# Kernel optimization log

Hardware: AMD Instinct MI355X
Metric: run time of the kernel (lower is better)

Reference implementation:

```python
import jax, jax.numpy as jnp
import numpy as np

B, S, NSAMP = 64, 21, 3000
HID, SEC, N, ATT = 500, 6, 2, 128
OUT, NPROTO, NCLS, NHEAD = 128, 25, 5, 4


def _pe(length, d):
    pos = np.arange(length, dtype=np.float32)[:, None]
    div = np.exp(np.arange(0, d, 2, dtype=np.float32) * (-np.log(10000.0) / d))
    pe = np.zeros((length, d), np.float32)
    pe[:, 0::2] = np.sin(pos * div)
    pe[:, 1::2] = np.cos(pos * div)
    return jnp.asarray(pe)


def _ln(x, g, b, eps=1e-5):
    m = x.mean(-1, keepdims=True)
    v = ((x - m) ** 2).mean(-1, keepdims=True)
    return (x - m) * jax.lax.rsqrt(v + eps) * g + b


def _conv1d(x, w, b):
    y = jax.lax.conv_general_dilated(x, w, (1,), [(1, 1)], dimension_numbers=('NCH', 'OIH', 'NCH'))
    return y + b[None, :, None]


def _maxpool(x, k):
    n, c, l = x.shape
    m = (l // k) * k  # torch MaxPool1d floors
    return x[:, :, :m].reshape(n, c, l // k, k).max(-1)


def _bn_eval(x, g, b, eps=1e-5):
    # eval-mode BatchNorm1d with running_mean=0, running_var=1
    return x * (g / np.sqrt(1.0 + eps))[None, :, None] + b[None, :, None]


def setup_inputs():
    key = jax.random.key(0)
    ks = jax.random.split(key, 16)
    def w(i, shape, s=0.02):
        return jax.random.normal(ks[i], shape, jnp.float32) * s
    u = jax.random.uniform(ks[0], (B * S * N, SEC), jnp.float32, 1e-6, 1.0 - 1e-6)
    return dict(
        x=jax.random.normal(ks[1], (B, S, 1, NSAMP), jnp.float32),
        gumbel=-jnp.log(-jnp.log(u)),
        wq=w(2, (HID, ATT * N)), wk=w(3, (HID, ATT * N)),
        w1=w(4, (32, 1, 3)), b1=jnp.zeros(32), bn1_g=jnp.ones(32), bn1_b=jnp.zeros(32),
        w2=w(5, (64, 32, 3)), b2=jnp.zeros(64), bn2_g=jnp.ones(64), bn2_b=jnp.zeros(64),
        w3=w(6, (128, 64, 3)), b3=jnp.zeros(128), bn3_g=jnp.ones(128), bn3_b=jnp.zeros(128),
        fc_w=w(7, (768, 256)), fc_b=jnp.zeros(256),
        fc2_w=w(8, (256, OUT)), fc2_b=jnp.zeros(OUT),
        protos=w(9, (NPROTO, OUT), 1.0),
        in_w=w(10, (OUT, 3 * OUT)), in_b=jnp.zeros(3 * OUT),
        out_w=w(11, (OUT, OUT)), out_b=jnp.zeros(OUT),
        ln1_g=jnp.ones(OUT), ln1_b=jnp.zeros(OUT),
        ln2_g=jnp.ones(OUT), ln2_b=jnp.zeros(OUT),
        ff1_w=w(12, (OUT, OUT)), ff1_b=jnp.zeros(OUT),
        ff2_w=w(13, (OUT, OUT)), ff2_b=jnp.zeros(OUT),
        clf_w=w(14, (OUT, NCLS)), clf_b=jnp.zeros(NCLS),
    )


def reference(x, gumbel, wq, wk, w1, b1, bn1_g, bn1_b, w2, b2, bn2_g, bn2_b,
              w3, b3, bn3_g, bn3_b, fc_w, fc_b, fc2_w, fc2_b, protos,
              in_w, in_b, out_w, out_b, ln1_g, ln1_b, ln2_g, ln2_b,
              ff1_w, ff1_b, ff2_w, ff2_b, clf_w, clf_b):
    bs = B * S
    # ---- HardAttentionLayer (gumbel hard sampling over SEC sections) ----
    xr = x.reshape(bs, SEC, HID)                       # (BS, 6, 500)
    xp = xr + _pe(100, HID)[None, :SEC]
    q = (xp @ wq).reshape(bs, SEC, N, ATT).transpose(0, 2, 1, 3)  # bnsh
    k = (xp @ wk).reshape(bs, SEC, N, ATT).transpose(0, 2, 1, 3)
    att = jnp.einsum('bnsh,bnth->bnst', q, k) / (HID ** 0.5)
    logits = (att.sum(-1) / SEC).reshape(bs * N, SEC)
    y_soft = jax.nn.softmax(logits + gumbel)           # tau = 1.0
    y_hard = jax.nn.one_hot(jnp.argmax(y_soft, -1), SEC, dtype=y_soft.dtype)
    alphas = (y_hard - jax.lax.stop_gradient(y_soft) + y_soft).reshape(bs, N, SEC)
    sampled = jnp.einsum('bns,bsh->bnh', alphas, xr)   # (BS, N, 500)
    # ---- conv/MLP epoch encoder (eval: dropout off, BN running stats) ----
    c = sampled.reshape(bs * N, 1, HID)
    c = _bn_eval(_maxpool(jax.nn.relu(_conv1d(c, w1, b1)), 4), bn1_g, bn1_b)
    c = _bn_eval(_maxpool(jax.nn.relu(_conv1d(c, w2, b2)), HID // 100), bn2_g, bn2_b)
    c = _bn_eval(_maxpool(jax.nn.relu(_conv1d(c, w3, b3)), 4), bn3_g, bn3_b)
    c = c.reshape(bs * N, -1) @ fc_w + fc_b
    z = c @ fc2_w + fc2_b                              # (B*S*N, 128)
    # ---- PrototypeLayer: VQ codebook lookup with straight-through ----
    d2 = (z * z).sum(1, keepdims=True) + (protos * protos).sum(1) - 2.0 * z @ protos.T
    proto = protos[jnp.argmin(d2, 1)]
    proto_st = z + jax.lax.stop_gradient(proto - z)
    # ---- SequenceEncoder: 1-layer post-norm transformer ----
    p_clf = proto_st.reshape(B, S, N, OUT).sum(2) / N  # (B, S, 128)
    h = p_clf + _pe(1024, OUT)[None, :S]
    qkv = h @ in_w + in_b
    qh, kh, vh = [t.reshape(B, S, NHEAD, OUT // NHEAD) for t in jnp.split(qkv, 3, -1)]
    sc = jnp.einsum('bqhd,bkhd->bhqk', qh, kh) / ((OUT // NHEAD) ** 0.5)
    ctx = jnp.einsum('bhqk,bkhd->bqhd', jax.nn.softmax(sc, -1), vh).reshape(B, S, OUT)
    h = _ln(h + ctx @ out_w + out_b, ln1_g, ln1_b)
    ff = jax.nn.relu(h @ ff1_w + ff1_b) @ ff2_w + ff2_b
    h = _ln(h + ff, ln2_g, ln2_b)
    return (h.reshape(-1, OUT) @ clf_w + clf_b).reshape(B, S, NCLS)
```

## Files before the change

### kernel.cpp

```cpp
#include <hip/hip_runtime.h>
#include <math.h>

#define BB 64
#define SS 21
#define NSAMP 3000
#define HID 500
#define SECN 6
#define NN 2
#define OUTD 128
#define NPROTO 25
#define NCLS 5
#define NHEAD 4
#define BS (BB*SS)
#define NSAMPLE (BS*NN)

#define C500 (-0.0184206807439523674f)
#define C128 (-0.07195578415606439f)
#define LSCALE 0.00745355992499929898f

#define WS_W2HI 5376
#define WS_W2LO 8448
#define WS_W3HI 11520
#define WS_W3LO 23808
#define WS_P3   36096
#define WS_C3   55296
#define WS_WQT  55424
#define WS_V    727424
#define WS_QKV  WS_V
#define WS_CTX  (WS_V + 520192)

typedef __attribute__((ext_vector_type(8))) short short8;
typedef __attribute__((ext_vector_type(4))) float floatx4;

__device__ __forceinline__ short f2bf(float f) {
  unsigned u = __float_as_uint(f);
  u += 0x7FFF + ((u >> 16) & 1);
  return (short)(u >> 16);
}
__device__ __forceinline__ float bf2f(short h) {
  return __uint_as_float(((unsigned)(unsigned short)h) << 16);
}

__global__ __launch_bounds__(256) void prep_all_kernel(
    const float* __restrict__ w2, const float* __restrict__ w3,
    short* __restrict__ w2hi, short* __restrict__ w2lo,
    short* __restrict__ w3hi, short* __restrict__ w3lo,
    const float* __restrict__ protos, const float* __restrict__ fc2w,
    const float* __restrict__ fcw, const float* __restrict__ fcb,
    const float* __restrict__ fc2b,
    float* __restrict__ P3, float* __restrict__ c3,
    const float* __restrict__ wq, float* __restrict__ wqT) {
  __shared__ __align__(16) float p2row[256];
  __shared__ float red[256];
  __shared__ float tile[64][65];
  const int t = threadIdx.x;
  if (blockIdx.x < 120) {
    int idx = blockIdx.x * 256 + t;
    if (idx < 6144) {
      int ic = idx & 31, ck = idx >> 5, k = ck % 3, c = ck / 3;
      float v = w2[c * 96 + ic * 3 + k];
      int dst = (((k * 4 + (c >> 4)) * 64) + ((ic >> 3) * 16 + (c & 15))) * 8 + (ic & 7);
      short hi = f2bf(v);
      short lo = f2bf(v - bf2f(hi));
      w2hi[dst] = hi; w2lo[dst] = lo;
    } else if (idx < 30720) {
      int j = idx - 6144;
      int ic = j & 63, ck = j >> 6, k = ck % 3, c = ck / 3;
      float v = w3[(c * 64 + ic) * 3 + k];
      int s = k * 2 + (ic >> 5);
      int dst = (((s * 8 + (c >> 4)) * 64) + (((ic & 31) >> 3) * 16 + (c & 15))) * 8 + (ic & 7);
      short hi = f2bf(v);
      short lo = f2bf(v - bf2f(hi));
      w3hi[dst] = hi; w3lo[dst] = lo;
    }
    return;
  }
  if (blockIdx.x >= 145) {
    int tid = blockIdx.x - 145;
    int h0 = (tid >> 2) * 64, c0 = (tid & 3) * 64;
    for (int e = t; e < 4096; e += 256) {
      int i = e >> 6, j = e & 63;
      if (h0 + i < 500) tile[j][i] = wq[(h0 + i) * 256 + c0 + j];
    }
    __syncthreads();
    for (int e = t; e < 4096; e += 256) {
      int c = e >> 6, hh = e & 63;
      if (h0 + hh < 500) wqT[(c0 + c) * 500 + h0 + hh] = tile[c][hh];
    }
    return;
  }
  const int p = blockIdx.x - 120, j = t;
  {
    const float4* pr = reinterpret_cast<const float4*>(protos + p * 128);
    const float4* wr = reinterpret_cast<const float4*>(fc2w + j * 128);
    float4 a4 = make_float4(0.f, 0.f, 0.f, 0.f);
    for (int c4 = 0; c4 < 32; c4++) {
      float4 a = pr[c4], b = wr[c4];
      a4.x += a.x * b.x; a4.y += a.y * b.y; a4.z += a.z * b.z; a4.w += a.w * b.w;
    }
    float v = (a4.x + a4.y) + (a4.z + a4.w);
    p2row[j] = v;
    float contrib = v * fcb[j];
    if (j < 128) {
      float pv = protos[p * 128 + j];
      contrib += pv * fc2b[j] - 0.5f * pv * pv;
    }
    red[j] = contrib;
  }
  __syncthreads();
  for (int s = 128; s > 0; s >>= 1) {
    if (j < s) red[j] += red[j + s];
    __syncthreads();
  }
  if (j == 0) c3[p] = red[0];
  for (int k = j; k < 768; k += 256) {
    const float4* fr = reinterpret_cast<const float4*>(fcw + k * 256);
    const float4* p2 = reinterpret_cast<const float4*>(p2row);
    float4 a4 = make_float4(0.f, 0.f, 0.f, 0.f);
    for (int j4 = 0; j4 < 64; j4++) {
      float4 a = p2[j4], b = fr[j4];
      a4.x += a.x * b.x; a4.y += a.y * b.y; a4.z += a.z * b.z; a4.w += a.w * b.w;
    }
    P3[p * 768 + k] = (a4.x + a4.y) + (a4.z + a4.w);
  }
}

#define MBX 4
__global__ __launch_bounds__(512) void attn_b_kernel(
    const float* __restrict__ x, const float* __restrict__ wk,
    const float* __restrict__ wqT, float* __restrict__ v) {
  __shared__ __align__(16) float pesum[500];
  __shared__ __align__(16) float xs[MBX * 500];
  __shared__ __align__(16) float ksp[2 * 256 * MBX];
  __shared__ __align__(16) float ks_t[256 * MBX];
  const int blk = blockIdx.x, t = threadIdx.x;

  if (t < 125) {
    float div0 = expf((float)(4 * t) * C500);
    float div1 = expf((float)(4 * t + 2) * C500);
    float s0 = 0.f, c0 = 0.f, s1 = 0.f, c1 = 0.f;
#pragma unroll
    for (int s = 0; s < SECN; s++) {
      float a0 = (float)s * div0, a1 = (float)s * div1;
      s0 += sinf(a0); c0 += cosf(a0);
      s1 += sinf(a1); c1 += cosf(a1);
    }
    reinterpret_cast<float4*>(pesum)[t] = make_float4(s0, c0, s1, c1);
  }
  __syncthreads();

  for (int e = t; e < MBX * 125; e += 512) {
    int m = e / 125, h4 = e % 125;
    const float4* xr = reinterpret_cast<const float4*>(x) + (blk * MBX + m) * 750;
    float4 a = xr[h4];
#pragma unroll
    for (int s = 1; s < SECN; s++) {
      float4 b = xr[s * 125 + h4];
      a.x += b.x; a.y += b.y; a.z += b.z; a.w += b.w;
    }
    float4 pe = reinterpret_cast<float4*>(pesum)[h4];
    a.x += pe.x; a.y += pe.y; a.z += pe.z; a.w += pe.w;
    reinterpret_cast<float4*>(xs)[m * 125 + h4] = a;
  }
  __syncthreads();

  {
    int c = t & 255, kh = t >> 8;
    float acc[MBX];
#pragma unroll
    for (int m = 0; m < MBX; m++) acc[m] = 0.f;
    int b4 = kh ? 63 : 0, e4 = kh ? 125 : 63;
    const float4* xsb = reinterpret_cast<const float4*>(xs);
    for (int i4 = b4; i4 < e4; i4++) {
      int i = i4 * 4;
      float w0 = wk[(i + 0) * 256 + c];
      float w1 = wk[(i + 1) * 256 + c];
      float w2 = wk[(i + 2) * 256 + c];
      float w3 = wk[(i + 3) * 256 + c];
#pragma unroll
      for (int m = 0; m < MBX; m++) {
        float4 xv = xsb[m * 125 + i4];
        acc[m] += xv.x * w0 + xv.y * w1 + xv.z * w2 + xv.w * w3;
      }
    }
#pragma unroll
    for (int m = 0; m < MBX; m++)
      ksp[(kh * 256 + c) * MBX + m] = acc[m];
  }
  __syncthreads();
  for (int e = t; e < 256 * MBX; e += 512) ks_t[e] = ksp[e] + ksp[256 * MBX + e];
  __syncthreads();

  if (t < 500) {
    int h = t;
#pragma unroll
    for (int n = 0; n < 2; n++) {
      float acc[MBX];
#pragma unroll
      for (int m = 0; m < MBX; m++) acc[m] = 0.f;
      const float* wcol = wqT + (n * 128) * 500 + h;
      const floatx4* ktb = (const floatx4*)ks_t + n * 128;
      for (int c = 0; c < 128; c++) {
        float w = wcol[c * 500];
        floatx4 k0 = ktb[c];
        acc[0] += w * k0[0]; acc[1] += w * k0[1]; acc[2] += w * k0[2]; acc[3] += w * k0[3];
      }
#pragma unroll
      for (int m = 0; m < MBX; m++)
        v[((blk * MBX + m) * 2 + n) * 500 + h] = acc[m];
    }
  }
}

__global__ __launch_bounds__(192) void attn_c_kernel(
    const float* __restrict__ x, const float* __restrict__ v,
    const float* __restrict__ gumbel, int* __restrict__ sec_idx) {
  __shared__ float lgsh[NN][SECN];
  const int bs = blockIdx.x, t = threadIdx.x;
  const int s = t >> 5, lane = t & 31;
  const float4* x4 = reinterpret_cast<const float4*>(x) + bs * 750 + s * 125;
  const float4* v0 = reinterpret_cast<const float4*>(v) + bs * 250;
  const float4* v1 = v0 + 125;
  float a0 = 0.f, a1 = 0.f;
  for (int h4 = lane; h4 < 125; h4 += 32) {
    float4 xv = x4[h4];
    float div0 = expf((float)(4 * h4) * C500);
    float div1 = expf((float)(4 * h4 + 2) * C500);
    float ang0 = (float)s * div0, ang1 = (float)s * div1;
    xv.x += sinf(ang0); xv.y += cosf(ang0);
    xv.z += sinf(ang1); xv.w += cosf(ang1);
    float4 w0 = v0[h4], w1 = v1[h4];
    a0 += xv.x * w0.x + xv.y * w0.y + xv.z * w0.z + xv.w * w0.w;
    a1 += xv.x * w1.x + xv.y * w1.y + xv.z * w1.z + xv.w * w1.w;
  }
#pragma unroll
  for (int m = 16; m >= 1; m >>= 1) {
    a0 += __shfl_xor(a0, m);
    a1 += __shfl_xor(a1, m);
  }
  if (lane == 0) {
    lgsh[0][s] = a0 * LSCALE + gumbel[(bs * 2 + 0) * SECN + s];
    lgsh[1][s] = a1 * LSCALE + gumbel[(bs * 2 + 1) * SECN + s];
  }
  __syncthreads();
  if (t < 2) {
    int best = 0; float bv = lgsh[t][0];
    for (int i = 1; i < SECN; i++) {
      float q = lgsh[t][i];
      if (q > bv) { bv = q; best = i; }
    }
    sec_idx[bs * 2 + t] = best;
  }
}

#define CONV_LDS 53568
__global__ __launch_bounds__(256, 3) void conv_kernel(
    const float* __restrict__ x, const int* __restrict__ sec_idx,
    const float* __restrict__ w1, const float* __restrict__ b1,
    const float* __restrict__ bn1g, const float* __restrict__ bn1b,
    const short* __restrict__ w2hi, const short* __restrict__ w2lo,
    const float* __restrict__ b2,
    const float* __restrict__ bn2g, const float* __restrict__ bn2b,
    const short* __restrict__ w3hi, const short* __restrict__ w3lo,
    const float* __restrict__ b3,
    const float* __restrict__ bn3g, const float* __restrict__ bn3b,
    const float* __restrict__ P3, const float* __restrict__ c3,
    int* __restrict__ proto_idx) {
  __shared__ __align__(16) char smem[CONV_LDS];
  short* act1_hi  = (short*)smem;
  short* act1_lo  = (short*)(smem + 10400);
  short* act2p_hi = (short*)smem;
  short* act2p_lo = (short*)(smem + 4896);
  float* featsh   = (float*)(smem + 9792);
  float* sc25     = (float*)(smem + 12864);
  float* in0p  = (float*)(smem + 20800);
  float* act2t = (float*)(smem + 20800);
  float* act3t = (float*)(smem + 20800);

  const int sample = blockIdx.x;
  const int t = threadIdx.x;
  const int bsIdx = sample >> 1;
  const float bnscale = rsqrtf(1.0f + 1e-5f);
  const int wv = t >> 6, l = t & 63, lr = l & 15, lg2 = l >> 4;

  {
    int sec = sec_idx[sample];
    const float* src = &x[bsIdx * NSAMP + sec * HID];
    for (int i = t; i < 512; i += 256) in0p[i] = (i >= 1 && i <= 500) ? src[i - 1] : 0.f;
    if (t < 200) {
      int r = t / 40; r = (r == 0) ? 0 : 125 + r;
      int idx = r * 40 + t % 40;
      act1_hi[idx] = 0; act1_lo[idx] = 0;
    }
  }
  __syncthreads();

  {
    int ic = t & 31;
    float w0 = w1[ic * 3], w1v = w1[ic * 3 + 1], w2v = w1[ic * 3 + 2];
    float bb = b1[ic];
    float g = bn1g[ic] * bnscale, be = bn1b[ic];
    for (int p = t >> 5; p < 125; p += 8) {
      int base = 4 * p;
      float xm1 = in0p[base], x0 = in0p[base + 1], x1 = in0p[base + 2],
            x2 = in0p[base + 3], x3 = in0p[base + 4], x4 = in0p[base + 5];
      float a0 = bb + w0 * xm1 + w1v * x0 + w2v * x1;
      float a1 = bb + w0 * x0  + w1v * x1 + w2v * x2;
      float a2 = bb + w0 * x1  + w1v * x2 + w2v * x3;
      float a3 = bb + w0 * x2  + w1v * x3 + w2v * x4;
      float m = fmaxf(fmaxf(fmaxf(fmaxf(a0, a1), a2), a3), 0.f);
      float v = m * g + be;
      short hi = f2bf(v);
      short lo = f2bf(v - bf2f(hi));
      act1_hi[(p + 1) * 40 + ic] = hi;
      act1_lo[(p + 1) * 40 + ic] = lo;
    }
  }
  __syncthreads();

  {
    floatx4 acc[4][2];
#pragma unroll
    for (int m = 0; m < 4; m++)
#pragma unroll
      for (int nn = 0; nn < 2; nn++) acc[m][nn] = (floatx4){0.f, 0.f, 0.f, 0.f};
#pragma unroll
    for (int s = 0; s < 3; s++) {
      short8 Ah[4], Al[4], Bh[2], Bl[2];
#pragma unroll
      for (int m = 0; m < 4; m++) {
        int aoff = ((s * 4 + m) * 64 + l) * 8;
        Ah[m] = *(const short8*)(w2hi + aoff);
        Al[m] = *(const short8*)(w2lo + aoff);
      }
#pragma unroll
      for (int nn = 0; nn < 2; nn++) {
        int boff = ((2 * wv + nn) * 16 + lr + s) * 40 + lg2 * 8;
        Bh[nn] = *(const short8*)(act1_hi + boff);
        Bl[nn] = *(const short8*)(act1_lo + boff);
      }
#pragma unroll
      for (int m = 0; m < 4; m++)
#pragma unroll
        for (int nn = 0; nn < 2; nn++) {
          acc[m][nn] = __builtin_amdgcn_mfma_f32_16x16x32_bf16(Ah[m], Bh[nn], acc[m][nn], 0, 0, 0);
          acc[m][nn] = __builtin_amdgcn_mfma_f32_16x16x32_bf16(Ah[m], Bl[nn], acc[m][nn], 0, 0, 0);
          acc[m][nn] = __builtin_amdgcn_mfma_f32_16x16x32_bf16(Al[m], Bh[nn], acc[m][nn], 0, 0, 0);
        }
    }
#pragma unroll
    for (int m = 0; m < 4; m++)
#pragma unroll
      for (int nn = 0; nn < 2; nn++) {
        int p = (2 * wv + nn) * 16 + lr;
        int swz = (m * 4 + lg2) ^ lr;
        *(floatx4*)(act2t + p * 64 + swz * 4) = acc[m][nn];
      }
  }
  __syncthreads();

  {
    if (t < 162) {
      for (int i = t; i < 648; i += 162) {
        int r = i / 72; r = (r == 0) ? 0 : 25 + r;
        int idx = r * 72 + i % 72;
        act2p_hi[idx] = 0; act2p_lo[idx] = 0;
      }
    }
    int ic = t & 63;
    float bb = b2[ic], g = bn2g[ic] * bnscale, be = bn2b[ic];
#define A2T(r, c) act2t[(r) * 64 + ((((c) >> 2) ^ ((r) & 15)) << 2) + ((c) & 3)]
    for (int pw = t >> 6; pw < 25; pw += 4) {
      int base = 5 * pw;
      float m = A2T(base, ic);
      m = fmaxf(m, A2T(base + 1, ic));
      m = fmaxf(m, A2T(base + 2, ic));
      m = fmaxf(m, A2T(base + 3, ic));
      m = fmaxf(m, A2T(base + 4, ic));
      float v = fmaxf(m + bb, 0.f) * g + be;
      short hi = f2bf(v);
      short lo = f2bf(v - bf2f(hi));
      act2p_hi[(pw + 1) * 72 + ic] = hi;
      act2p_lo[(pw + 1) * 72 + ic] = lo;
    }
#undef A2T
  }
  __syncthreads();

  {
    floatx4 acc[2][2];
#pragma unroll
    for (int mm = 0; mm < 2; mm++)
#pragma unroll
      for (int nn = 0; nn < 2; nn++) acc[mm][nn] = (floatx4){0.f, 0.f, 0.f, 0.f};
#pragma unroll
    for (int s = 0; s < 6; s++) {
      short8 Ah[2], Al[2], Bh[2], Bl[2];
#pragma unroll
      for (int mm = 0; mm < 2; mm++) {
        int aoff = ((s * 8 + (wv * 2 + mm)) * 64 + l) * 8;
        Ah[mm] = *(const short8*)(w3hi + aoff);
        Al[mm] = *(const short8*)(w3lo + aoff);
      }
#pragma unroll
      for (int nn = 0; nn < 2; nn++) {
        int boff = (nn * 16 + lr + (s >> 1)) * 72 + (s & 1) * 32 + lg2 * 8;
        Bh[nn] = *(const short8*)(act2p_hi + boff);
        Bl[nn] = *(const short8*)(act2p_lo + boff);
      }
#pragma unroll
      for (int mm = 0; mm < 2; mm++)
#pragma unroll
        for (int nn = 0; nn < 2; nn++) {
          acc[mm][nn] = __builtin_amdgcn_mfma_f32_16x16x32_bf16(Ah[mm], Bh[nn], acc[mm][nn], 0, 0, 0);
          acc[mm][nn] = __builtin_amdgcn_mfma_f32_16x16x32_bf16(Ah[mm], Bl[nn], acc[mm][nn], 0, 0, 0);
          acc[mm][nn] = __builtin_amdgcn_mfma_f32_16x16x32_bf16(Al[mm], Bh[nn], acc[mm][nn], 0, 0, 0);
        }
    }
#pragma unroll
    for (int mm = 0; mm < 2; mm++)
#pragma unroll
      for (int nn = 0; nn < 2; nn++) {
        int p = nn * 16 + lr;
        *(floatx4*)(act3t + p * 132 + (wv * 2 + mm) * 16 + lg2 * 4) = acc[mm][nn];
      }
  }
  __syncthreads();

  {
    int c = t & 127;
    float bb = b3[c], g = bn3g[c] * bnscale, be = bn3b[c];
    for (int pw = t >> 7; pw < 6; pw += 2) {
      int base = 4 * pw;
      float m = act3t[base * 132 + c];
      m = fmaxf(m, act3t[(base + 1) * 132 + c]);
      m = fmaxf(m, act3t[(base + 2) * 132 + c]);
      m = fmaxf(m, act3t[(base + 3) * 132 + c]);
      float v = fmaxf(m + bb, 0.f) * g + be;
      featsh[c * 6 + pw] = v;
    }
  }
  __syncthreads();

  if (t < NPROTO * 8) {
    int p = t >> 3, part = t & 7;
    const float4* pr = reinterpret_cast<const float4*>(P3 + p * 768 + part * 96);
    const float4* fr = reinterpret_cast<const float4*>(featsh + part * 96);
    float4 a4 = make_float4(0.f, 0.f, 0.f, 0.f);
#pragma unroll
    for (int i = 0; i < 24; i++) {
      float4 w = pr[i], f = fr[i];
      a4.x += w.x * f.x; a4.y += w.y * f.y; a4.z += w.z * f.z; a4.w += w.w * f.w;
    }
    float a = (a4.x + a4.y) + (a4.z + a4.w);
    a += __shfl_xor(a, 1);
    a += __shfl_xor(a, 2);
    a += __shfl_xor(a, 4);
    if (part == 0) sc25[p] = a + c3[p];
  }
  __syncthreads();
  if (t == 0) {
    int best = 0; float bv = sc25[0];
    for (int i = 1; i < NPROTO; i++) {
      float v = sc25[i];
      if (v > bv) { bv = v; best = i; }
    }
    proto_idx[sample] = best;
  }
}

__global__ __launch_bounds__(384) void seq_qkv_kernel(
    const int* __restrict__ proto_idx, const float* __restrict__ protos,
    const float* __restrict__ inw, const float* __restrict__ inb,
    float* __restrict__ qkv) {
  __shared__ __align__(16) float hrow[OUTD];
  const int bs = blockIdx.x, t = threadIdx.x;
  const int s = bs % SS;
  if (t < OUTD) {
    int i0 = proto_idx[bs * 2], i1 = proto_idx[bs * 2 + 1];
    float pc = 0.5f * (protos[i0 * OUTD + t] + protos[i1 * OUTD + t]);
    float div = expf((float)(2 * (t >> 1)) * C128);
    float ang = (float)s * div;
    float pe = (t & 1) ? cosf(ang) : sinf(ang);
    hrow[t] = pc + pe;
  }
  __syncthreads();
  float a = inb[t];
  const float4* hr = reinterpret_cast<const float4*>(hrow);
  for (int d4 = 0; d4 < 32; d4++) {
    float4 h4 = hr[d4];
    int d = d4 * 4;
    a += h4.x * inw[(d + 0) * 384 + t] + h4.y * inw[(d + 1) * 384 + t]
       + h4.z * inw[(d + 2) * 384 + t] + h4.w * inw[(d + 3) * 384 + t];
  }
  qkv[bs * 384 + t] = a;
}

__global__ __launch_bounds__(256) void seq_attn_kernel(
    const float* __restrict__ qkv, float* __restrict__ ctxbuf) {
  __shared__ float qs_[SS][32], ks_[SS][32], vs_[SS][32];
  __shared__ float sc_[SS][SS + 1];
  const int b = blockIdx.x >> 2, hd = blockIdx.x & 3;
  const int t = threadIdx.x;
  for (int e = t; e < SS * 32; e += 256) {
    int s = e >> 5, dd = e & 31;
    const float* base = qkv + (b * SS + s) * 384 + hd * 32 + dd;
    qs_[s][dd] = base[0];
    ks_[s][dd] = base[128];
    vs_[s][dd] = base[256];
  }
  __syncthreads();
  for (int e = t; e < SS * SS; e += 256) {
    int qs = e / SS, ks = e % SS;
    float a = 0.f;
#pragma unroll
    for (int d = 0; d < 32; d++) a += qs_[qs][d] * ks_[ks][d];
    sc_[qs][ks] = a * 0.17677669529663689f;
  }
  __syncthreads();
  if (t < SS) {
    float mx = sc_[t][0];
    for (int i = 1; i < SS; i++) mx = fmaxf(mx, sc_[t][i]);
    float sum = 0.f;
    for (int i = 0; i < SS; i++) { float e = expf(sc_[t][i] - mx); sc_[t][i] = e; sum += e; }
    float inv = 1.f / sum;
    for (int i = 0; i < SS; i++) sc_[t][i] *= inv;
  }
  __syncthreads();
  for (int e = t; e < SS * 32; e += 256) {
    int qs = e >> 5, dd = e & 31;
    float a = 0.f;
#pragma unroll
    for (int ks = 0; ks < SS; ks++) a += sc_[qs][ks] * vs_[ks][dd];
    ctxbuf[(b * SS + qs) * OUTD + hd * 32 + dd] = a;
  }
}

__global__ __launch_bounds__(128) void seq_tail_kernel(
    const int* __restrict__ proto_idx, const float* __restrict__ protos,
    const float* __restrict__ ctxbuf,
    const float* __restrict__ outw, const float* __restrict__ outb,
    const float* __restrict__ ln1g, const float* __restrict__ ln1b,
    const float* __restrict__ ff1w, const float* __restrict__ ff1b,
    const float* __restrict__ ff2w, const float* __restrict__ ff2b,
    const float* __restrict__ ln2g, const float* __restrict__ ln2b,
    const float* __restrict__ clfw, const float* __restrict__ clfb,
    float* __restrict__ out) {
  __shared__ __align__(16) float rowA[OUTD];
  __shared__ __align__(16) float rowB[OUTD];
  __shared__ float lds2[2];
  const int bs = blockIdx.x, t = threadIdx.x;
  const int s = bs % SS;

  rowA[t] = ctxbuf[bs * OUTD + t];
  __syncthreads();
  float a = outb[t];
  {
    const float4* cr = reinterpret_cast<const float4*>(rowA);
    for (int e4 = 0; e4 < 32; e4++) {
      float4 c4 = cr[e4];
      int e = e4 * 4;
      a += c4.x * outw[(e + 0) * OUTD + t] + c4.y * outw[(e + 1) * OUTD + t]
         + c4.z * outw[(e + 2) * OUTD + t] + c4.w * outw[(e + 3) * OUTD + t];
    }
  }
  float hv;
  {
    int i0 = proto_idx[bs * 2], i1 = proto_idx[bs * 2 + 1];
    float pc = 0.5f * (protos[i0 * OUTD + t] + protos[i1 * OUTD + t]);
    float div = expf((float)(2 * (t >> 1)) * C128);
    float ang = (float)s * div;
    float pe = (t & 1) ? cosf(ang) : sinf(ang);
    hv = pc + pe;
  }
  float tmp = hv + a;
  {
    float v = tmp;
#pragma unroll
    for (int k = 32; k >= 1; k >>= 1) v += __shfl_xor(v, k);
    if ((t & 63) == 0) lds2[t >> 6] = v;
    __syncthreads();
    float m = (lds2[0] + lds2[1]) * (1.0f / OUTD);
    __syncthreads();
    float u = tmp - m;
    float w = u * u;
#pragma unroll
    for (int k = 32; k >= 1; k >>= 1) w += __shfl_xor(w, k);
    if ((t & 63) == 0) lds2[t >> 6] = w;
    __syncthreads();
    float var = (lds2[0] + lds2[1]) * (1.0f / OUTD);
    __syncthreads();
    rowA[t] = u * rsqrtf(var + 1e-5f) * ln1g[t] + ln1b[t];
  }
  __syncthreads();
  {
    float r = ff1b[t];
    const float4* hr = reinterpret_cast<const float4*>(rowA);
    for (int e4 = 0; e4 < 32; e4++) {
      float4 h4 = hr[e4];
      int e = e4 * 4;
      r += h4.x * ff1w[(e + 0) * OUTD + t] + h4.y * ff1w[(e + 1) * OUTD + t]
         + h4.z * ff1w[(e + 2) * OUTD + t] + h4.w * ff1w[(e + 3) * OUTD + t];
    }
    rowB[t] = fmaxf(r, 0.f);
  }
  __syncthreads();
  float tmp2;
  {
    float r = ff2b[t];
    const float4* cr = reinterpret_cast<const float4*>(rowB);
    for (int e4 = 0; e4 < 32; e4++) {
      float4 c4 = cr[e4];
      int e = e4 * 4;
      r += c4.x * ff2w[(e + 0) * OUTD + t] + c4.y * ff2w[(e + 1) * OUTD + t]
         + c4.z * ff2w[(e + 2) * OUTD + t] + c4.w * ff2w[(e + 3) * OUTD + t];
    }
    tmp2 = rowA[t] + r;
  }
  __syncthreads();
  {
    float v = tmp2;
#pragma unroll
    for (int k = 32; k >= 1; k >>= 1) v += __shfl_xor(v, k);
    if ((t & 63) == 0) lds2[t >> 6] = v;
    __syncthreads();
    float m = (lds2[0] + lds2[1]) * (1.0f / OUTD);
    __syncthreads();
    float u = tmp2 - m;
    float w = u * u;
#pragma unroll
    for (int k = 32; k >= 1; k >>= 1) w += __shfl_xor(w, k);
    if ((t & 63) == 0) lds2[t >> 6] = w;
    __syncthreads();
    float var = (lds2[0] + lds2[1]) * (1.0f / OUTD);
    rowA[t] = u * rsqrtf(var + 1e-5f) * ln2g[t] + ln2b[t];
  }
  __syncthreads();
  if (t < NCLS) {
    float acc = clfb[t];
    for (int d = 0; d < OUTD; d++) acc += rowA[d] * clfw[d * NCLS + t];
    out[bs * NCLS + t] = acc;
  }
}

extern "C" void kernel_launch(void* const* d_in, const int* in_sizes, int n_in,
                              void* d_out, int out_size, void* d_ws, size_t ws_size,
                              hipStream_t stream) {
  const float* x     = (const float*)d_in[0];
  const float* gum   = (const float*)d_in[1];
  const float* wq    = (const float*)d_in[2];
  const float* wk    = (const float*)d_in[3];
  const float* w1    = (const float*)d_in[4];
  const float* b1    = (const float*)d_in[5];
  const float* bn1g  = (const float*)d_in[6];
  const float* bn1b  = (const float*)d_in[7];
  const float* w2    = (const float*)d_in[8];
  const float* b2    = (const float*)d_in[9];
  const float* bn2g  = (const float*)d_in[10];
  const float* bn2b  = (const float*)d_in[11];
  const float* w3    = (const float*)d_in[12];
  const float* b3    = (const float*)d_in[13];
  const float* bn3g  = (const float*)d_in[14];
  const float* bn3b  = (const float*)d_in[15];
  const float* fcw   = (const float*)d_in[16];
  const float* fcb   = (const float*)d_in[17];
  const float* fc2w  = (const float*)d_in[18];
  const float* fc2b  = (const float*)d_in[19];
  const float* prot  = (const float*)d_in[20];
  const float* inw   = (const float*)d_in[21];
  const float* inb   = (const float*)d_in[22];
  const float* outw  = (const float*)d_in[23];
  const float* outb  = (const float*)d_in[24];
  const float* ln1g  = (const float*)d_in[25];
  const float* ln1b  = (const float*)d_in[26];
  const float* ln2g  = (const float*)d_in[27];
  const float* ln2b  = (const float*)d_in[28];
  const float* ff1w  = (const float*)d_in[29];
  const float* ff1b  = (const float*)d_in[30];
  const float* ff2w  = (const float*)d_in[31];
  const float* ff2b  = (const float*)d_in[32];
  const float* clfw  = (const float*)d_in[33];
  const float* clfb  = (const float*)d_in[34];
  float* out = (float*)d_out;

  int* sec_idx   = (int*)d_ws;
  int* proto_idx = sec_idx + NSAMPLE;
  short* w2hi = (short*)((float*)d_ws + WS_W2HI);
  short* w2lo = (short*)((float*)d_ws + WS_W2LO);
  short* w3hi = (short*)((float*)d_ws + WS_W3HI);
  short* w3lo = (short*)((float*)d_ws + WS_W3LO);
  float* P3   = (float*)d_ws + WS_P3;
  float* c3   = (float*)d_ws + WS_C3;
  float* wqT  = (float*)d_ws + WS_WQT;
  float* vbuf = (float*)d_ws + WS_V;
  float* qkv  = (float*)d_ws + WS_QKV;
  float* ctxb = (float*)d_ws + WS_CTX;

  hipLaunchKernelGGL(prep_all_kernel, dim3(177), dim3(256), 0, stream,
                     w2, w3, w2hi, w2lo, w3hi, w3lo,
                     prot, fc2w, fcw, fcb, fc2b, P3, c3, wq, wqT);
  hipLaunchKernelGGL(attn_b_kernel, dim3(BS / MBX), dim3(512), 0, stream,
                     x, wk, wqT, vbuf);
  hipLaunchKernelGGL(attn_c_kernel, dim3(BS), dim3(192), 0, stream,
                     x, vbuf, gum, sec_idx);
  hipLaunchKernelGGL(conv_kernel, dim3(NSAMPLE), dim3(256), 0, stream,
                     x, sec_idx, w1, b1, bn1g, bn1b, w2hi, w2lo, b2, bn2g, bn2b,
                     w3hi, w3lo, b3, bn3g, bn3b, P3, c3, proto_idx);
  hipLaunchKernelGGL(seq_qkv_kernel, dim3(BS), dim3(384), 0, stream,
                     proto_idx, prot, inw, inb, qkv);
  hipLaunchKernelGGL(seq_attn_kernel, dim3(BB * NHEAD), dim3(256), 0, stream,
                     qkv, ctxb);
  hipLaunchKernelGGL(seq_tail_kernel, dim3(BS), dim3(128), 0, stream,
                     proto_idx, prot, ctxb, outw, outb, ln1g, ln1b,
                     ff1w, ff1b, ff2w, ff2b, ln2g, ln2b, clfw, clfb, out);
}
```

Baseline: 184.5 us.

## Double conv kernel block to 512 threads, splitting MFMA tiles across more waves

Grows the per-sample conv kernel from 4 to 8 wavefronts. Each wave in the conv2 and conv3 MFMA stages now owns one output tile instead of two, and the strided elementwise loops are adjusted to match. The aim is more parallelism and latency hiding per block, with fewer accumulators per thread. In exchange, weight fragments are loaded by more waves, and each block still uses about 53 KB of LDS, which may cap how many 512-thread blocks fit per CU. The requested launch bounds of 6 blocks per CU may not be reachable.

```diff
diff --git a/kernel.cpp b/kernel.cpp
--- a/kernel.cpp
+++ b/kernel.cpp
@@ -254,7 +254,7 @@
 }
 
 #define CONV_LDS 53568
-__global__ __launch_bounds__(256, 3) void conv_kernel(
+__global__ __launch_bounds__(512, 6) void conv_kernel(
     const float* __restrict__ x, const int* __restrict__ sec_idx,
     const float* __restrict__ w1, const float* __restrict__ b1,
     const float* __restrict__ bn1g, const float* __restrict__ bn1b,
@@ -286,7 +286,7 @@
   {
     int sec = sec_idx[sample];
     const float* src = &x[bsIdx * NSAMP + sec * HID];
-    for (int i = t; i < 512; i += 256) in0p[i] = (i >= 1 && i <= 500) ? src[i - 1] : 0.f;
+    if (t < 512) in0p[t] = (t >= 1 && t <= 500) ? src[t - 1] : 0.f;
     if (t < 200) {
       int r = t / 40; r = (r == 0) ? 0 : 125 + r;
       int idx = r * 40 + t % 40;
@@ -300,7 +300,7 @@
     float w0 = w1[ic * 3], w1v = w1[ic * 3 + 1], w2v = w1[ic * 3 + 2];
     float bb = b1[ic];
     float g = bn1g[ic] * bnscale, be = bn1b[ic];
-    for (int p = t >> 5; p < 125; p += 8) {
+    for (int p = t >> 5; p < 125; p += 16) {
       int base = 4 * p;
       float xm1 = in0p[base], x0 = in0p[base + 1], x1 = in0p[base + 2],
             x2 = in0p[base + 3], x3 = in0p[base + 4], x4 = in0p[base + 5];
@@ -319,43 +319,36 @@
   __syncthreads();
 
   {
-    floatx4 acc[4][2];
-#pragma unroll
-    for (int m = 0; m < 4; m++)
-#pragma unroll
-      for (int nn = 0; nn < 2; nn++) acc[m][nn] = (floatx4){0.f, 0.f, 0.f, 0.f};
+    floatx4 acc[4];
+#pragma unroll
+    for (int m = 0; m < 4; m++) acc[m] = (floatx4){0.f, 0.f, 0.f, 0.f};
 #pragma unroll
     for (int s = 0; s < 3; s++) {
-      short8 Ah[4], Al[4], Bh[2], Bl[2];
+      short8 Ah[4], Al[4], Bh, Bl;
 #pragma unroll
       for (int m = 0; m < 4; m++) {
         int aoff = ((s * 4 + m) * 64 + l) * 8;
         Ah[m] = *(const short8*)(w2hi + aoff);
         Al[m] = *(const short8*)(w2lo + aoff);
       }
-#pragma unroll
-      for (int nn = 0; nn < 2; nn++) {
-        int boff = ((2 * wv + nn) * 16 + lr + s) * 40 + lg2 * 8;
-        Bh[nn] = *(const short8*)(act1_hi + boff);
-        Bl[nn] = *(const short8*)(act1_lo + boff);
-      }
-#pragma unroll
-      for (int m = 0; m < 4; m++)
-#pragma unroll
-        for (int nn = 0; nn < 2; nn++) {
-          acc[m][nn] = __builtin_amdgcn_mfma_f32_16x16x32_bf16(Ah[m], Bh[nn], acc[m][nn], 0, 0, 0);
-          acc[m][nn] = __builtin_amdgcn_mfma_f32_16x16x32_bf16(Ah[m], Bl[nn], acc[m][nn], 0, 0, 0);
-          acc[m][nn] = __builtin_amdgcn_mfma_f32_16x16x32_bf16(Al[m], Bh[nn], acc[m][nn], 0, 0, 0);
-        }
-    }
-#pragma unroll
-    for (int m = 0; m < 4; m++)
-#pragma unroll
-      for (int nn = 0; nn < 2; nn++) {
-        int p = (2 * wv + nn) * 16 + lr;
-        int swz = (m * 4 + lg2) ^ lr;
-        *(floatx4*)(act2t + p * 64 + swz * 4) = acc[m][nn];
-      }
+      {
+        int boff = (wv * 16 + lr + s) * 40 + lg2 * 8;
+        Bh = *(const short8*)(act1_hi + boff);
+        Bl = *(const short8*)(act1_lo + boff);
+      }
+#pragma unroll
+      for (int m = 0; m < 4; m++) {
+        acc[m] = __builtin_amdgcn_mfma_f32_16x16x32_bf16(Ah[m], Bh, acc[m], 0, 0, 0);
+        acc[m] = __builtin_amdgcn_mfma_f32_16x16x32_bf16(Ah[m], Bl, acc[m], 0, 0, 0);
+        acc[m] = __builtin_amdgcn_mfma_f32_16x16x32_bf16(Al[m], Bh, acc[m], 0, 0, 0);
+      }
+    }
+#pragma unroll
+    for (int m = 0; m < 4; m++) {
+      int p = wv * 16 + lr;
+      int swz = (m * 4 + lg2) ^ lr;
+      *(floatx4*)(act2t + p * 64 + swz * 4) = acc[m];
+    }
   }
   __syncthreads();
 
@@ -370,7 +363,7 @@
     int ic = t & 63;
     float bb = b2[ic], g = bn2g[ic] * bnscale, be = bn2b[ic];
 #define A2T(r, c) act2t[(r) * 64 + ((((c) >> 2) ^ ((r) & 15)) << 2) + ((c) & 3)]
-    for (int pw = t >> 6; pw < 25; pw += 4) {
+    for (int pw = t >> 6; pw < 25; pw += 8) {
       int base = 5 * pw;
       float m = A2T(base, ic);
       m = fmaxf(m, A2T(base + 1, ic));
@@ -388,19 +381,16 @@
   __syncthreads();
 
   {
-    floatx4 acc[2][2];
-#pragma unroll
-    for (int mm = 0; mm < 2; mm++)
-#pragma unroll
-      for (int nn = 0; nn < 2; nn++) acc[mm][nn] = (floatx4){0.f, 0.f, 0.f, 0.f};
+    floatx4 acc[2];
+#pragma unroll
+    for (int nn = 0; nn < 2; nn++) acc[nn] = (floatx4){0.f, 0.f, 0.f, 0.f};
 #pragma unroll
     for (int s = 0; s < 6; s++) {
-      short8 Ah[2], Al[2], Bh[2], Bl[2];
-#pragma unroll
-      for (int mm = 0; mm < 2; mm++) {
-        int aoff = ((s * 8 + (wv * 2 + mm)) * 64 + l) * 8;
-        Ah[mm] = *(const short8*)(w3hi + aoff);
-        Al[mm] = *(const short8*)(w3lo + aoff);
+      short8 Ah, Al, Bh[2], Bl[2];
+      {
+        int aoff = ((s * 8 + wv) * 64 + l) * 8;
+        Ah = *(const short8*)(w3hi + aoff);
+        Al = *(const short8*)(w3lo + aoff);
       }
 #pragma unroll
       for (int nn = 0; nn < 2; nn++) {
@@ -409,28 +399,24 @@
         Bl[nn] = *(const short8*)(act2p_lo + boff);
       }
 #pragma unroll
-      for (int mm = 0; mm < 2; mm++)
-#pragma unroll
-        for (int nn = 0; nn < 2; nn++) {
-          acc[mm][nn] = __builtin_amdgcn_mfma_f32_16x16x32_bf16(Ah[mm], Bh[nn], acc[mm][nn], 0, 0, 0);
-          acc[mm][nn] = __builtin_amdgcn_mfma_f32_16x16x32_bf16(Ah[mm], Bl[nn], acc[mm][nn], 0, 0, 0);
-          acc[mm][nn] = __builtin_amdgcn_mfma_f32_16x16x32_bf16(Al[mm], Bh[nn], acc[mm][nn], 0, 0, 0);
-        }
-    }
-#pragma unroll
-    for (int mm = 0; mm < 2; mm++)
-#pragma unroll
       for (int nn = 0; nn < 2; nn++) {
-        int p = nn * 16 + lr;
-        *(floatx4*)(act3t + p * 132 + (wv * 2 + mm) * 16 + lg2 * 4) = acc[mm][nn];
-      }
+        acc[nn] = __builtin_amdgcn_mfma_f32_16x16x32_bf16(Ah, Bh[nn], acc[nn], 0, 0, 0);
+        acc[nn] = __builtin_amdgcn_mfma_f32_16x16x32_bf16(Ah, Bl[nn], acc[nn], 0, 0, 0);
+        acc[nn] = __builtin_amdgcn_mfma_f32_16x16x32_bf16(Al, Bh[nn], acc[nn], 0, 0, 0);
+      }
+    }
+#pragma unroll
+    for (int nn = 0; nn < 2; nn++) {
+      int p = nn * 16 + lr;
+      *(floatx4*)(act3t + p * 132 + wv * 16 + lg2 * 4) = acc[nn];
+    }
   }
   __syncthreads();
 
   {
     int c = t & 127;
     float bb = b3[c], g = bn3g[c] * bnscale, be = bn3b[c];
-    for (int pw = t >> 7; pw < 6; pw += 2) {
+    for (int pw = t >> 7; pw < 6; pw += 4) {
       int base = 4 * pw;
       float m = act3t[base * 132 + c];
       m = fmaxf(m, act3t[(base + 1) * 132 + c]);
@@ -703,7 +689,7 @@
                      x, wk, wqT, vbuf);
   hipLaunchKernelGGL(attn_c_kernel, dim3(BS), dim3(192), 0, stream,
                      x, vbuf, gum, sec_idx);
-  hipLaunchKernelGGL(conv_kernel, dim3(NSAMPLE), dim3(256), 0, stream,
+  hipLaunchKernelGGL(conv_kernel, dim3(NSAMPLE), dim3(512), 0, stream,
                      x, sec_idx, w1, b1, bn1g, bn1b, w2hi, w2lo, b2, bn2g, bn2b,
                      w3hi, w3lo, b3, bn3g, bn3b, P3, c3, proto_idx);
   hipLaunchKernelGGL(seq_qkv_kernel, dim3(BS), dim3(384), 0, stream,
```

After: 183.1 us. Within noise of the previous version (-0.8%).
